# Performance work log

Measured on AMD Instinct MI355X. Metric: run time of the kernel, lower is better.

Reference implementation:

```python
import jax, jax.numpy as jnp
import numpy as np

L, N, E, H, R = 2048, 4, 768, 12, 16
ALPHA = 16.0
LORA_SCALE = ALPHA / R
HEAD_DIM = E // H


def setup_inputs() -> dict:
    rng = jax.random.key(0)
    ks = jax.random.split(rng, 15)
    g = lambda i, shape, s=1.0: jax.random.normal(ks[i], shape, jnp.float32) * s
    return {
        "query": g(0, (L, N, E)),
        "key": g(1, (L, N, E)),
        "value": g(2, (L, N, E)),
        "in_proj_weight": g(3, (3 * E, E), 0.02),
        "in_proj_bias": g(4, (3 * E,), 0.02),
        "q_down": g(5, (R, E), 0.02),
        "q_up": g(6, (E, R), 0.02),
        "k_down": g(7, (R, E), 0.02),
        "k_up": g(8, (E, R), 0.02),
        "v_down": g(9, (R, E), 0.02),
        "v_up": g(10, (E, R), 0.02),
        "out_proj_weight": g(11, (E, E), 0.02),
        "out_proj_bias": g(12, (E,), 0.02),
        "out_down": g(13, (R, E), 0.02),
        "out_up": g(14, (E, R), 0.02),
    }


def _lora_linear(x, W, b, down, up):
    # y = x W^T + b + scale * (x down^T) up^T   (LoRA-adapted nn.Linear)
    return x @ W.T + b + LORA_SCALE * ((x @ down.T) @ up.T)


def reference(query, key, value, in_proj_weight, in_proj_bias,
              q_down, q_up, k_down, k_up, v_down, v_up,
              out_proj_weight, out_proj_bias, out_down, out_up):
    Wq, Wk, Wv = jnp.split(in_proj_weight, 3, axis=0)
    bq, bk, bv = jnp.split(in_proj_bias, 3)
    q = _lora_linear(query, Wq, bq, q_down, q_up)   # (L,N,E)
    k = _lora_linear(key, Wk, bk, k_down, k_up)     # (S,N,E)
    v = _lora_linear(value, Wv, bv, v_down, v_up)

    def to_heads(t):  # (T,N,E) -> (N,H,T,hd)
        return t.reshape(t.shape[0], N, H, HEAD_DIM).transpose(1, 2, 0, 3)

    qh, kh, vh = to_heads(q), to_heads(k), to_heads(v)
    scale = 1.0 / jnp.sqrt(jnp.float32(HEAD_DIM))
    scores = jnp.einsum('nhld,nhsd->nhls', qh * scale, kh)  # (N,H,L,S)
    attn = jax.nn.softmax(scores, axis=-1)
    o = jnp.einsum('nhls,nhsd->nhld', attn, vh)             # (N,H,L,hd)
    o = o.transpose(2, 0, 1, 3).reshape(L, N, E)            # (L,N,E)
    return _lora_linear(o, out_proj_weight, out_proj_bias, out_down, out_up)
```

## Files before the change

### kernel.cpp

```cpp
#include <hip/hip_runtime.h>

#define LL 2048
#define NN 4
#define EE 768
#define HH 12
#define RR 16
#define HD 64
#define TT (LL*NN)
#define F3 (3*EE)

typedef __bf16 bf16;
typedef bf16 bf16x4 __attribute__((ext_vector_type(4)));
typedef bf16 bf16x8 __attribute__((ext_vector_type(8)));
typedef float floatx4 __attribute__((ext_vector_type(4)));
typedef float floatx16 __attribute__((ext_vector_type(16)));
typedef unsigned uintx4 __attribute__((ext_vector_type(4)));

#define ZERO16 (floatx16){0.f,0.f,0.f,0.f,0.f,0.f,0.f,0.f,0.f,0.f,0.f,0.f,0.f,0.f,0.f,0.f}

__device__ __forceinline__ unsigned pk_bf16(float a, float b) {
    unsigned r;
    asm("v_cvt_pk_bf16_f32 %0, %1, %2" : "=v"(r) : "v"(a), "v"(b));
    return r;
}

__global__ __launch_bounds__(256) void prep_w(
    const float* __restrict__ W,  const float* __restrict__ qu,
    const float* __restrict__ ku, const float* __restrict__ vu,
    const float* __restrict__ Wo, const float* __restrict__ ou,
    const float* __restrict__ qd, const float* __restrict__ kd,
    const float* __restrict__ vd, const float* __restrict__ odw,
    bf16* __restrict__ Wa)
{
    const int f0 = blockIdx.x * 16;
    const int tid = threadIdx.x;

    const float* Wsrc;
    const float* up;
    const float* dn;
    if (f0 < F3) {
        const int third = f0 / EE, fe = f0 % EE;
        Wsrc = W + (size_t)f0*EE;
        up   = ((third == 0) ? qu : (third == 1) ? ku : vu) + (size_t)fe*RR;
        dn   = (third == 0) ? qd : (third == 1) ? kd : vd;
    } else {
        const int fe = f0 - F3;
        Wsrc = Wo + (size_t)fe*EE;
        up   = ou + (size_t)fe*RR;
        dn   = odw;
    }

    float dnv[3][RR];
    #pragma unroll
    for (int i = 0; i < 3; ++i)
        #pragma unroll
        for (int r = 0; r < RR; ++r)
            dnv[i][r] = dn[(size_t)r*EE + i*256 + tid];

    for (int fr = 0; fr < 16; ++fr) {
        float u[RR];
        #pragma unroll
        for (int r = 0; r < RR; ++r) u[r] = up[(size_t)fr*RR + r];
        bf16* orow = Wa + (size_t)(f0 + fr)*EE;
        #pragma unroll
        for (int i = 0; i < 3; ++i) {
            float acc = Wsrc[(size_t)fr*EE + i*256 + tid];
            #pragma unroll
            for (int r = 0; r < RR; ++r) acc += u[r] * dnv[i][r];
            orow[i*256 + tid] = (bf16)acc;
        }
    }
}

template<int MODE>
__global__ __launch_bounds__(256, 3) void gemm_aug(
    const float* __restrict__ Aq, const float* __restrict__ Ak,
    const float* __restrict__ Av, const bf16* __restrict__ Abf,
    const bf16* __restrict__ B,
    const float* __restrict__ bias,
    bf16* __restrict__ qo, bf16* __restrict__ ko, bf16* __restrict__ vo,
    float* __restrict__ fo)
{
    __shared__ bf16 As[128][72];
    __shared__ bf16 Bs[128][72];
    const int t0 = blockIdx.x * 128;
    const int f0 = blockIdx.y * 128;
    const int tid = threadIdx.x;
    const int wave = tid >> 6, lane = tid & 63;
    const int quad = lane >> 4, l16 = lane & 15;
    const int m0 = (wave & 1) * 64;
    const int n0 = (wave >> 1) * 64;

    const int third = (MODE == 0) ? (f0 / EE) : 0;
    const float* A32 = (MODE == 0)
        ? ((third == 0) ? Aq : (third == 1) ? Ak : Av) : nullptr;

    const int r0 = tid >> 3, cg = tid & 7;

    float4 ga0[4], ga1[4];
    bf16x8 gab[4];
    bf16x8 gbb[4];

#define LOADT(kb) do {                                                        \
        _Pragma("unroll")                                                     \
        for (int c = 0; c < 4; ++c) {                                         \
            if constexpr (MODE == 0) {                                        \
                const float* src =                                            \
                    A32 + (size_t)(t0 + c*32 + r0)*EE + (kb)*64 + cg*8;       \
                ga0[c] = *(const float4*)(src);                               \
                ga1[c] = *(const float4*)(src + 4);                           \
            } else {                                                          \
                gab[c] = *(const bf16x8*)(                                    \
                    Abf + (size_t)(t0 + c*32 + r0)*EE + (kb)*64 + cg*8);      \
            }                                                                 \
            gbb[c] = *(const bf16x8*)(                                        \
                B + (size_t)(f0 + c*32 + r0)*EE + (kb)*64 + cg*8);            \
        }                                                                     \
    } while (0)
#define STORET() do {                                                         \
        _Pragma("unroll")                                                     \
        for (int c = 0; c < 4; ++c) {                                         \
            if constexpr (MODE == 0) {                                        \
                union { uintx4 u; bf16x8 h; } cv;                             \
                cv.u = (uintx4){ pk_bf16(ga0[c].x, ga0[c].y),                 \
                                 pk_bf16(ga0[c].z, ga0[c].w),                 \
                                 pk_bf16(ga1[c].x, ga1[c].y),                 \
                                 pk_bf16(ga1[c].z, ga1[c].w) };               \
                *(bf16x8*)(&As[c*32 + r0][cg*8]) = cv.h;                      \
            } else {                                                          \
                *(bf16x8*)(&As[c*32 + r0][cg*8]) = gab[c];                    \
            }                                                                 \
            *(bf16x8*)(&Bs[c*32 + r0][cg*8]) = gbb[c];                        \
        }                                                                     \
    } while (0)

    floatx4 acc[4][4];
    #pragma unroll
    for (int rt = 0; rt < 4; ++rt)
        #pragma unroll
        for (int ct = 0; ct < 4; ++ct) acc[rt][ct] = (floatx4){0.f,0.f,0.f,0.f};

    LOADT(0);
    STORET();
    __syncthreads();

    for (int kb = 0; kb < EE/64; ++kb) {
        if (kb + 1 < EE/64) LOADT(kb + 1);
        #pragma unroll
        for (int kc = 0; kc < 2; ++kc) {
            bf16x8 a[4], bfr[4];
            #pragma unroll
            for (int rt = 0; rt < 4; ++rt)
                a[rt] = *(const bf16x8*)(&As[m0 + rt*16 + l16][kc*32 + quad*8]);
            #pragma unroll
            for (int ct = 0; ct < 4; ++ct)
                bfr[ct] = *(const bf16x8*)(&Bs[n0 + ct*16 + l16][kc*32 + quad*8]);
            #pragma unroll
            for (int rt = 0; rt < 4; ++rt)
                #pragma unroll
                for (int ct = 0; ct < 4; ++ct)
                    acc[rt][ct] = __builtin_amdgcn_mfma_f32_16x16x32_bf16(
                        a[rt], bfr[ct], acc[rt][ct], 0, 0, 0);
        }
        __syncthreads();
        if (kb + 1 < EE/64) {
            STORET();
            __syncthreads();
        }
    }
#undef LOADT
#undef STORET

    #pragma unroll
    for (int rt = 0; rt < 4; ++rt) {
        #pragma unroll
        for (int r = 0; r < 4; ++r) {
            const int t = t0 + m0 + rt*16 + quad*4 + r;
            #pragma unroll
            for (int ct = 0; ct < 4; ++ct) {
                const int fl = n0 + ct*16 + l16;
                float c = acc[rt][ct][r] + bias[f0 + fl];
                if (MODE == 0) {
                    const int fe = (f0 % EE) + fl;
                    const int h = fe >> 6, d = fe & 63;
                    const int l = t >> 2, n = t & 3;
                    const size_t idx = (((size_t)(n*HH + h)*LL) + l)*HD + d;
                    if (third == 0)      qo[idx] = (bf16)(c * 0.180336877f);
                    else if (third == 1) ko[idx] = (bf16)c;
                    else                 vo[idx] = (bf16)c;
                } else {
                    fo[(size_t)t*EE + f0 + fl] = c;
                }
            }
        }
    }
}

__global__ __launch_bounds__(256) void vtrans(
    const bf16* __restrict__ vin, bf16* __restrict__ vout)
{
    __shared__ bf16 T[64][64];
    const int nh = blockIdx.x >> 5;
    const int l0 = (blockIdx.x & 31) * 64;
    const int tid = threadIdx.x;
    const bf16* src = vin + ((size_t)nh*LL + l0)*HD;
    #pragma unroll
    for (int c = 0; c < 2; ++c) {
        int id = c*256 + tid;
        int row = id >> 3, dg = id & 7;
        int pg = dg ^ (row & 7);
        *(bf16x8*)(&T[row][pg*8]) = *(const bf16x8*)(src + row*HD + dg*8);
    }
    __syncthreads();
    bf16* dst = vout + (size_t)nh*HD*LL;
    const int wave = tid >> 6, lane = tid & 63;
    #pragma unroll
    for (int it = 0; it < 2; ++it) {
        const int d  = it*32 + wave*8 + (lane >> 3);
        const int cg = lane & 7;
        bf16x8 vv;
        #pragma unroll
        for (int j = 0; j < 8; ++j) {
            const int lrow = cg*8 + j;
            const int pg = (d >> 3) ^ (lrow & 7);
            vv[j] = T[lrow][pg*8 + (d & 7)];
        }
        *(bf16x8*)(dst + (size_t)d*LL + l0 + cg*8) = vv;
    }
}

__device__ __forceinline__ void compute_tile(
    const bf16 (&KS)[64][64], const bf16 (&VS)[64][64],
    const bf16x8 (&bq)[4], const bf16x8& ones, const floatx16& z16,
    int l32, int hi, int sw,
    floatx16& oacc0, floatx16& oacc1, floatx16& oaccS)
{
    #pragma unroll
    for (int ss = 0; ss < 2; ++ss) {
        bf16x8 ak[4];
        #pragma unroll
        for (int t4 = 0; t4 < 4; ++t4)
            ak[t4] = *(const bf16x8*)(&KS[ss*32 + l32][((t4*2 + hi) ^ sw) * 8]);

        __builtin_amdgcn_s_setprio(1);
        floatx16 sacc = __builtin_amdgcn_mfma_f32_32x32x16_bf16(
            ak[0], bq[0], z16, 0, 0, 0);
        #pragma unroll
        for (int t4 = 1; t4 < 4; ++t4)
            sacc = __builtin_amdgcn_mfma_f32_32x32x16_bf16(
                ak[t4], bq[t4], sacc, 0, 0, 0);
        __builtin_amdgcn_s_setprio(0);

        bf16x8 bv[4];
        #pragma unroll
        for (int tl = 0; tl < 2; ++tl)
            #pragma unroll
            for (int dt = 0; dt < 2; ++dt)
                bv[tl*2 + dt] = *(const bf16x8*)(
                    &VS[dt*32 + l32][((ss*4 + tl*2 + hi) ^ sw) * 8]);

        float p[16];
        #pragma unroll
        for (int r = 0; r < 16; ++r) p[r] = __builtin_amdgcn_exp2f(sacc[r]);

        union { uintx4 u; bf16x8 h; } fr0, fr1;
        {
            unsigned c0 = pk_bf16(p[0], p[1]);
            unsigned c1 = pk_bf16(p[2], p[3]);
            unsigned c2 = pk_bf16(p[4], p[5]);
            unsigned c3 = pk_bf16(p[6], p[7]);
            asm("v_permlane32_swap_b32 %0, %1" : "+v"(c0), "+v"(c2));
            asm("v_permlane32_swap_b32 %0, %1" : "+v"(c1), "+v"(c3));
            fr0.u = (uintx4){c0, c1, c2, c3};
        }
        {
            unsigned c0 = pk_bf16(p[8],  p[9]);
            unsigned c1 = pk_bf16(p[10], p[11]);
            unsigned c2 = pk_bf16(p[12], p[13]);
            unsigned c3 = pk_bf16(p[14], p[15]);
            asm("v_permlane32_swap_b32 %0, %1" : "+v"(c0), "+v"(c2));
            asm("v_permlane32_swap_b32 %0, %1" : "+v"(c1), "+v"(c3));
            fr1.u = (uintx4){c0, c1, c2, c3};
        }

        __builtin_amdgcn_s_setprio(1);
        oaccS = __builtin_amdgcn_mfma_f32_32x32x16_bf16(fr0.h, ones, oaccS, 0, 0, 0);
        oaccS = __builtin_amdgcn_mfma_f32_32x32x16_bf16(fr1.h, ones, oaccS, 0, 0, 0);
        oacc0 = __builtin_amdgcn_mfma_f32_32x32x16_bf16(fr0.h, bv[0], oacc0, 0, 0, 0);
        oacc1 = __builtin_amdgcn_mfma_f32_32x32x16_bf16(fr0.h, bv[1], oacc1, 0, 0, 0);
        oacc0 = __builtin_amdgcn_mfma_f32_32x32x16_bf16(fr1.h, bv[2], oacc0, 0, 0, 0);
        oacc1 = __builtin_amdgcn_mfma_f32_32x32x16_bf16(fr1.h, bv[3], oacc1, 0, 0, 0);
        __builtin_amdgcn_s_setprio(0);
    }
}

__global__ __launch_bounds__(256, 3) void attn_mfma(
    const bf16* __restrict__ qf, const bf16* __restrict__ kf,
    const bf16* __restrict__ vf, bf16* __restrict__ Oa)
{
    __shared__ bf16 KsA[64][64], VtA[64][64];
    __shared__ bf16 KsB[64][64], VtB[64][64];

    const int bid = blockIdx.x;
    const int nh = bid % 48;
    const int l0 = (bid / 48) * 128;
    const int tid  = threadIdx.x;
    const int wave = tid >> 6;
    const int lane = tid & 63;
    const int l32  = lane & 31;
    const int hi   = lane >> 5;
    const int sw   = l32 & 7;

    const bf16* qb = qf + (size_t)nh * LL * HD;
    const bf16* kb = kf + (size_t)nh * LL * HD;
    const bf16* vb = vf + (size_t)nh * HD * LL;

    const int q0 = l0 + wave * 32;

    const int rowA = tid >> 3;
    const int rowB = rowA + 32;
    const int g0   = tid & 7;
    const int gsA  = g0 ^ (rowA & 7);

    const bf16* pK0 = kb + (size_t)rowA*HD + g0*8;
    const bf16* pK1 = kb + (size_t)rowB*HD + g0*8;
    const bf16* pV0 = vb + (size_t)rowA*LL + g0*8;
    const bf16* pV1 = vb + (size_t)rowB*LL + g0*8;

    bf16x8 bq[4];
    #pragma unroll
    for (int t = 0; t < 4; ++t)
        bq[t] = *(const bf16x8*)(qb + (size_t)(q0 + l32)*HD + t*16 + hi*8);

    const bf16x8 ones = { (bf16)1.f, (bf16)1.f, (bf16)1.f, (bf16)1.f,
                          (bf16)1.f, (bf16)1.f, (bf16)1.f, (bf16)1.f };
    const floatx16 z16 = ZERO16;

    floatx16 oacc0 = ZERO16;
    floatx16 oacc1 = ZERO16;
    floatx16 oaccS = ZERO16;

    bf16x8 gk0, gk1, gv0, gv1;

#define LOADT(S) do {                                                         \
        gk0 = *(const bf16x8*)(pK0 + (size_t)(S)*HD);                         \
        gk1 = *(const bf16x8*)(pK1 + (size_t)(S)*HD);                         \
        gv0 = *(const bf16x8*)(pV0 + (S));                                    \
        gv1 = *(const bf16x8*)(pV1 + (S));                                    \
    } while (0)
#define STORE_A() do {                                                        \
        *(bf16x8*)(&KsA[rowA][gsA*8]) = gk0;                                  \
        *(bf16x8*)(&KsA[rowB][gsA*8]) = gk1;                                  \
        *(bf16x8*)(&VtA[rowA][gsA*8]) = gv0;                                  \
        *(bf16x8*)(&VtA[rowB][gsA*8]) = gv1;                                  \
    } while (0)
#define STORE_B() do {                                                        \
        *(bf16x8*)(&KsB[rowA][gsA*8]) = gk0;                                  \
        *(bf16x8*)(&KsB[rowB][gsA*8]) = gk1;                                  \
        *(bf16x8*)(&VtB[rowA][gsA*8]) = gv0;                                  \
        *(bf16x8*)(&VtB[rowB][gsA*8]) = gv1;                                  \
    } while (0)

    LOADT(0);
    STORE_A();
    LOADT(64);
    __syncthreads();

    for (int tt = 0; tt < 16; ++tt) {
        STORE_B();
        LOADT((size_t)((2*tt + 2) & 31) * 64);
        compute_tile(KsA, VtA, bq, ones, z16, l32, hi, sw, oacc0, oacc1, oaccS);
        __syncthreads();
        STORE_A();
        LOADT((size_t)((2*tt + 3) & 31) * 64);
        compute_tile(KsB, VtB, bq, ones, z16, l32, hi, sw, oacc0, oacc1, oaccS);
        __syncthreads();
    }
#undef LOADT
#undef STORE_A
#undef STORE_B

    const int n = nh / HH, h = nh % HH;
    #pragma unroll
    for (int r = 0; r < 16; ++r) {
        const int qloc = (r & 3) + 8*(r >> 2) + 4*hi;
        const float iv = 1.f / oaccS[r];
        const size_t t = (size_t)(q0 + qloc)*NN + n;
        Oa[t*EE + h*64 + l32]      = (bf16)(oacc0[r] * iv);
        Oa[t*EE + h*64 + 32 + l32] = (bf16)(oacc1[r] * iv);
    }
}

extern "C" void kernel_launch(void* const* d_in, const int* in_sizes, int n_in,
                              void* d_out, int out_size, void* d_ws, size_t ws_size,
                              hipStream_t stream) {
    const float* q   = (const float*)d_in[0];
    const float* k   = (const float*)d_in[1];
    const float* v   = (const float*)d_in[2];
    const float* W   = (const float*)d_in[3];
    const float* b   = (const float*)d_in[4];
    const float* qd  = (const float*)d_in[5];
    const float* qu  = (const float*)d_in[6];
    const float* kd  = (const float*)d_in[7];
    const float* ku  = (const float*)d_in[8];
    const float* vd  = (const float*)d_in[9];
    const float* vu  = (const float*)d_in[10];
    const float* Wo  = (const float*)d_in[11];
    const float* bo  = (const float*)d_in[12];
    const float* odw = (const float*)d_in[13];
    const float* ou  = (const float*)d_in[14];
    float* out = (float*)d_out;

    char* wsb = (char*)d_ws;
    bf16* vfb = (bf16*)wsb;
    bf16* Oa  = (bf16*)(wsb + (size_t)TT*EE*2);
    bf16* Wa  = (bf16*)(wsb + (size_t)3*TT*EE*2);
    bf16* qfb = Wa + (size_t)3072*EE;
    bf16* kfb = qfb + (size_t)TT*EE;
    bf16* vld = kfb + (size_t)TT*EE;

    prep_w<<<192, 256, 0, stream>>>(W, qu, ku, vu, Wo, ou, qd, kd, vd, odw, Wa);
    gemm_aug<0><<<dim3(TT/128, F3/128), 256, 0, stream>>>(
        q, k, v, nullptr, Wa, b, qfb, kfb, vld, nullptr);
    vtrans<<<48*32, 256, 0, stream>>>(vld, vfb);
    attn_mfma<<<48*16, 256, 0, stream>>>(qfb, kfb, vfb, Oa);
    gemm_aug<1><<<dim3(TT/128, EE/128), 256, 0, stream>>>(
        nullptr, nullptr, nullptr, Oa, Wa + (size_t)F3*EE, bo,
        nullptr, nullptr, nullptr, out);
}
```

Baseline: 275.3 us.

## Double-buffer LDS tiles with XOR swizzle in projection GEMM

```diff
diff --git a/kernel.cpp b/kernel.cpp
--- a/kernel.cpp
+++ b/kernel.cpp
@@ -73,7 +73,7 @@
 }
 
 template<int MODE>
-__global__ __launch_bounds__(256, 3) void gemm_aug(
+__global__ __launch_bounds__(256, 2) void gemm_aug(
     const float* __restrict__ Aq, const float* __restrict__ Ak,
     const float* __restrict__ Av, const bf16* __restrict__ Abf,
     const bf16* __restrict__ B,
@@ -81,8 +81,8 @@
     bf16* __restrict__ qo, bf16* __restrict__ ko, bf16* __restrict__ vo,
     float* __restrict__ fo)
 {
-    __shared__ bf16 As[128][72];
-    __shared__ bf16 Bs[128][72];
+    __shared__ bf16 AsA[128][64], BsA[128][64];
+    __shared__ bf16 AsB[128][64], BsB[128][64];
     const int t0 = blockIdx.x * 128;
     const int f0 = blockIdx.y * 128;
     const int tid = threadIdx.x;
@@ -90,12 +90,14 @@
     const int quad = lane >> 4, l16 = lane & 15;
     const int m0 = (wave & 1) * 64;
     const int n0 = (wave >> 1) * 64;
+    const int swr = l16 & 7;
 
     const int third = (MODE == 0) ? (f0 / EE) : 0;
     const float* A32 = (MODE == 0)
         ? ((third == 0) ? Aq : (third == 1) ? Ak : Av) : nullptr;
 
     const int r0 = tid >> 3, cg = tid & 7;
+    const int gsw = cg ^ (r0 & 7);
 
     float4 ga0[4], ga1[4];
     bf16x8 gab[4];
@@ -117,7 +119,7 @@
                 B + (size_t)(f0 + c*32 + r0)*EE + (kb)*64 + cg*8);            \
         }                                                                     \
     } while (0)
-#define STORET() do {                                                         \
+#define STORET(AS, BS) do {                                                   \
         _Pragma("unroll")                                                     \
         for (int c = 0; c < 4; ++c) {                                         \
             if constexpr (MODE == 0) {                                        \
@@ -126,13 +128,33 @@
                                  pk_bf16(ga0[c].z, ga0[c].w),                 \
                                  pk_bf16(ga1[c].x, ga1[c].y),                 \
                                  pk_bf16(ga1[c].z, ga1[c].w) };               \
-                *(bf16x8*)(&As[c*32 + r0][cg*8]) = cv.h;                      \
+                *(bf16x8*)(&AS[c*32 + r0][gsw*8]) = cv.h;                     \
             } else {                                                          \
-                *(bf16x8*)(&As[c*32 + r0][cg*8]) = gab[c];                    \
+                *(bf16x8*)(&AS[c*32 + r0][gsw*8]) = gab[c];                   \
             }                                                                 \
-            *(bf16x8*)(&Bs[c*32 + r0][cg*8]) = gbb[c];                        \
+            *(bf16x8*)(&BS[c*32 + r0][gsw*8]) = gbb[c];                       \
         }                                                                     \
     } while (0)
+#define COMPUTE(AS, BS) do {                                                  \
+        _Pragma("unroll")                                                     \
+        for (int kc = 0; kc < 2; ++kc) {                                      \
+            bf16x8 a[4], bfr[4];                                              \
+            _Pragma("unroll")                                                 \
+            for (int rt = 0; rt < 4; ++rt)                                    \
+                a[rt] = *(const bf16x8*)(                                     \
+                    &AS[m0 + rt*16 + l16][((kc*4 + quad) ^ swr) * 8]);        \
+            _Pragma("unroll")                                                 \
+            for (int ct = 0; ct < 4; ++ct)                                    \
+                bfr[ct] = *(const bf16x8*)(                                   \
+                    &BS[n0 + ct*16 + l16][((kc*4 + quad) ^ swr) * 8]);        \
+            _Pragma("unroll")                                                 \
+            for (int rt = 0; rt < 4; ++rt)                                    \
+                _Pragma("unroll")                                             \
+                for (int ct = 0; ct < 4; ++ct)                                \
+                    acc[rt][ct] = __builtin_amdgcn_mfma_f32_16x16x32_bf16(    \
+                        a[rt], bfr[ct], acc[rt][ct], 0, 0, 0);                \
+        }                                                                     \
+    } while (0)
 
     floatx4 acc[4][4];
     #pragma unroll
@@ -140,36 +162,25 @@
         #pragma unroll
         for (int ct = 0; ct < 4; ++ct) acc[rt][ct] = (floatx4){0.f,0.f,0.f,0.f};
 
+    const int NT = EE/64;
     LOADT(0);
-    STORET();
+    STORET(AsA, BsA);
+    LOADT(1);
     __syncthreads();
 
-    for (int kb = 0; kb < EE/64; ++kb) {
-        if (kb + 1 < EE/64) LOADT(kb + 1);
-        #pragma unroll
-        for (int kc = 0; kc < 2; ++kc) {
-            bf16x8 a[4], bfr[4];
-            #pragma unroll
-            for (int rt = 0; rt < 4; ++rt)
-                a[rt] = *(const bf16x8*)(&As[m0 + rt*16 + l16][kc*32 + quad*8]);
-            #pragma unroll
-            for (int ct = 0; ct < 4; ++ct)
-                bfr[ct] = *(const bf16x8*)(&Bs[n0 + ct*16 + l16][kc*32 + quad*8]);
-            #pragma unroll
-            for (int rt = 0; rt < 4; ++rt)
-                #pragma unroll
-                for (int ct = 0; ct < 4; ++ct)
-                    acc[rt][ct] = __builtin_amdgcn_mfma_f32_16x16x32_bf16(
-                        a[rt], bfr[ct], acc[rt][ct], 0, 0, 0);
-        }
+    for (int tt = 0; tt < NT/2; ++tt) {
+        STORET(AsB, BsB);
+        { int k2 = 2*tt + 2; if (k2 >= NT) k2 -= NT; LOADT(k2); }
+        COMPUTE(AsA, BsA);
         __syncthreads();
-        if (kb + 1 < EE/64) {
-            STORET();
-            __syncthreads();
-        }
+        STORET(AsA, BsA);
+        { int k3 = 2*tt + 3; if (k3 >= NT) k3 -= NT; LOADT(k3); }
+        COMPUTE(AsB, BsB);
+        __syncthreads();
     }
 #undef LOADT
 #undef STORET
+#undef COMPUTE
 
     #pragma unroll
     for (int rt = 0; rt < 4; ++rt) {
```

Result: no change. 277.0 us (+0.6%).
